# Performance work log

Hardware: AMD Instinct MI355X
Metric: run time of the kernel (lower is better)

The kernel has to match this reference:

```python
import jax, jax.numpy as jnp
import numpy as np

BETA = 1.0
B, N, D = 2048, 131072, 256

def setup_inputs() -> dict:
    key = jax.random.key(0)
    k1, k2 = jax.random.split(key)
    x = jax.random.normal(k1, (B, D), dtype=jnp.float32)
    stored = jax.random.normal(k2, (N, D), dtype=jnp.float32)
    return {"x": x, "stored": stored}

def reference(x, stored):
    # scores: [B, N] = beta * x @ stored^T
    scores = BETA * jnp.einsum('bd,nd->bn', x, stored)
    attn = jax.nn.softmax(scores, axis=-1)
    # retrieved patterns: [B, D]
    return jnp.einsum('bn,nd->bd', attn, stored)
```

## Files before the change

### kernel.cpp

```cpp
#include <hip/hip_runtime.h>
#include <hip/hip_bf16.h>
#include <math.h>

#define B_Q 2048
#define N_K 131072
#define D_DIM 256
#define NCHUNK 32
#define CHUNK_KEYS (N_K / NCHUNK)
#define KTILE 32
#define NITER (CHUNK_KEYS / KTILE)
#define NTILES (N_K / KTILE)
#define TILE_USHORTS 16384

typedef __attribute__((ext_vector_type(8))) _Float16 half8;
typedef __attribute__((ext_vector_type(8))) short bf16x8;
typedef __attribute__((ext_vector_type(4))) float f32x4;

static __device__ __forceinline__ unsigned short f2bf(float f) {
    unsigned u = __builtin_bit_cast(unsigned, f);
    unsigned r = (u + 0x7fffu + ((u >> 16) & 1u)) >> 16;
    return (unsigned short)r;
}

typedef const __attribute__((address_space(1))) unsigned int* gas_p;
typedef __attribute__((address_space(3))) unsigned int* las_p;
static __device__ __forceinline__ void gl_lds16(const void* g, void* l) {
    __builtin_amdgcn_global_load_lds((gas_p)g, (las_p)l, 16, 0, 0);
}

__global__ __launch_bounds__(256) void prepass(const float* __restrict__ stored,
                                               unsigned short* __restrict__ frag) {
    __shared__ float sh[32][270];
    const int tid = threadIdx.x;
    const int t = blockIdx.x;
    const float* src = stored + (size_t)t * 32 * 256;
#pragma unroll
    for (int i = 0; i < 16; ++i) {
        int gi = i * 256 + tid;
        int row = gi >> 7, c2 = (gi & 127) << 1;
        *(float2*)&sh[row][c2] = *(const float2*)(src + row * 256 + c2);
    }
    __syncthreads();
    unsigned short* out = frag + (size_t)t * TILE_USHORTS;
#pragma unroll
    for (int i = 0; i < 4; ++i) {
        int ck = i * 256 + tid;
        int lane = ck & 63, col = lane & 15, quad = lane >> 4;
        int kg = ck >> 9, s = (ck >> 6) & 7;
        int key = kg * 16 + col, d0 = s * 32 + quad * 8;
        union { uint4 v; _Float16 e[8]; } o;
#pragma unroll
        for (int j2 = 0; j2 < 4; ++j2) {
            float2 f = *(const float2*)&sh[key][d0 + j2 * 2];
            o.e[j2 * 2]     = (_Float16)f.x;
            o.e[j2 * 2 + 1] = (_Float16)f.y;
        }
        *(uint4*)(out + ck * 8) = o.v;
    }
#pragma unroll
    for (int i = 0; i < 4; ++i) {
        int cv = i * 256 + tid;
        int lane = cv & 63, col = lane & 15, quad = lane >> 4;
        int dn = cv >> 6;
        int d = dn * 16 + col;
        union { uint4 v; unsigned short e[8]; } o;
#pragma unroll
        for (int j = 0; j < 8; ++j) o.e[j] = f2bf(sh[quad * 8 + j][d]);
        *(uint4*)(out + 8192 + cv * 8) = o.v;
    }
}

__global__ __launch_bounds__(256, 2)
void hopfield_main(const float* __restrict__ x,
                   const unsigned short* __restrict__ frag,
                   float* __restrict__ partO,
                   float* __restrict__ partl) {
    __shared__ __align__(16) unsigned short Kb[2][8192];
    __shared__ __align__(16) unsigned short Vb[2][8192];
    __shared__ __align__(16) unsigned short Pb[4][32][40];

    const int tid = threadIdx.x;
    const int wave = tid >> 6, lane = tid & 63;
    const int col = lane & 15, quad = lane >> 4;
    const int blk = blockIdx.x;
    const int chunk = blk & 31, qb = blk >> 5;
    const int q0w = qb * 128 + wave * 32;
    const unsigned short* fbase = frag + (size_t)chunk * NITER * TILE_USHORTS;

    half8 xf[2][8];
    float ss[2] = {0.f, 0.f};
#pragma unroll
    for (int qg = 0; qg < 2; ++qg) {
        const float* xr = x + (size_t)(q0w + qg * 16 + col) * 256;
#pragma unroll
        for (int s = 0; s < 8; ++s) {
            f32x4 a = *(const f32x4*)(xr + s * 32 + quad * 8);
            f32x4 b = *(const f32x4*)(xr + s * 32 + quad * 8 + 4);
            union { half8 v; _Float16 e[8]; } h;
#pragma unroll
            for (int j = 0; j < 4; ++j) {
                h.e[j] = (_Float16)a[j]; h.e[4 + j] = (_Float16)b[j];
                ss[qg] += a[j] * a[j] + b[j] * b[j];
            }
            xf[qg][s] = h.v;
        }
    }
#pragma unroll
    for (int qg = 0; qg < 2; ++qg) {
        ss[qg] += __shfl_xor(ss[qg], 16);
        ss[qg] += __shfl_xor(ss[qg], 32);
    }
    float M0q[2] = {4.9f * sqrtf(ss[0]), 4.9f * sqrtf(ss[1])};
    float M0v[2][4];
#pragma unroll
    for (int qg = 0; qg < 2; ++qg)
#pragma unroll
        for (int r = 0; r < 4; ++r)
            M0v[qg][r] = __shfl(M0q[qg], quad * 4 + r);

    f32x4 O[2][16];
#pragma unroll
    for (int qg = 0; qg < 2; ++qg)
#pragma unroll
        for (int dn = 0; dn < 16; ++dn) O[qg][dn] = (f32x4){0.f, 0.f, 0.f, 0.f};
    float lacc[2][4] = {{0.f, 0.f, 0.f, 0.f}, {0.f, 0.f, 0.f, 0.f}};

#pragma unroll
    for (int j = 0; j < 4; ++j) {
        int off = (wave * 4 + j) * 512 + lane * 8;
        gl_lds16(fbase + off, &Kb[0][off]);
        gl_lds16(fbase + 8192 + off, &Vb[0][off]);
    }

#pragma unroll 1
    for (int it = 0; it < NITER; ++it) {
        const int cur = it & 1;
        __syncthreads();

        const int itn = (it + 1 < NITER) ? it + 1 : it;
        const unsigned short* nbase = fbase + (size_t)itn * TILE_USHORTS;
#pragma unroll
        for (int j = 0; j < 4; ++j) {
            int off = (wave * 4 + j) * 512 + lane * 8;
            gl_lds16(nbase + off, &Kb[itn & 1][off]);
            gl_lds16(nbase + 8192 + off, &Vb[itn & 1][off]);
        }

        const unsigned short* K = Kb[cur];
        const unsigned short* V = Vb[cur];

        f32x4 S[2][2];
#pragma unroll
        for (int qg = 0; qg < 2; ++qg)
#pragma unroll
            for (int kg = 0; kg < 2; ++kg) S[qg][kg] = (f32x4){0.f, 0.f, 0.f, 0.f};
#pragma unroll
        for (int s = 0; s < 8; ++s) {
            half8 b0 = *(const half8*)(K + ((0 * 8 + s) * 64 + lane) * 8);
            half8 b1 = *(const half8*)(K + ((1 * 8 + s) * 64 + lane) * 8);
            S[0][0] = __builtin_amdgcn_mfma_f32_16x16x32_f16(xf[0][s], b0, S[0][0], 0, 0, 0);
            S[1][0] = __builtin_amdgcn_mfma_f32_16x16x32_f16(xf[1][s], b0, S[1][0], 0, 0, 0);
            S[0][1] = __builtin_amdgcn_mfma_f32_16x16x32_f16(xf[0][s], b1, S[0][1], 0, 0, 0);
            S[1][1] = __builtin_amdgcn_mfma_f32_16x16x32_f16(xf[1][s], b1, S[1][1], 0, 0, 0);
        }

        unsigned short* Pw = &Pb[wave][0][0];
#pragma unroll
        for (int qg = 0; qg < 2; ++qg)
#pragma unroll
            for (int r = 0; r < 4; ++r) {
                float m0 = M0v[qg][r];
                float p0 = __expf(S[qg][0][r] - m0);
                float p1 = __expf(S[qg][1][r] - m0);
                lacc[qg][r] += p0 + p1;
                int row = qg * 16 + quad * 4 + r;
                Pw[row * 40 + col]      = f2bf(p0);
                Pw[row * 40 + 16 + col] = f2bf(p1);
            }
        asm volatile("s_waitcnt lgkmcnt(0)" ::: "memory");
        bf16x8 pa[2];
#pragma unroll
        for (int qg = 0; qg < 2; ++qg)
            pa[qg] = *(const bf16x8*)&Pb[wave][qg * 16 + col][quad * 8];

#pragma unroll
        for (int dn = 0; dn < 16; ++dn) {
            bf16x8 bv = *(const bf16x8*)(V + (dn * 64 + lane) * 8);
            O[0][dn] = __builtin_amdgcn_mfma_f32_16x16x32_bf16(pa[0], bv, O[0][dn], 0, 0, 0);
            O[1][dn] = __builtin_amdgcn_mfma_f32_16x16x32_bf16(pa[1], bv, O[1][dn], 0, 0, 0);
        }
    }

#pragma unroll
    for (int qg = 0; qg < 2; ++qg)
#pragma unroll
        for (int r = 0; r < 4; ++r) {
            float v = lacc[qg][r];
            v += __shfl_xor(v, 1); v += __shfl_xor(v, 2);
            v += __shfl_xor(v, 4); v += __shfl_xor(v, 8);
            if (col == 0)
                partl[(size_t)chunk * B_Q + q0w + qg * 16 + quad * 4 + r] = v;
        }
#pragma unroll
    for (int qg = 0; qg < 2; ++qg)
#pragma unroll
        for (int dn = 0; dn < 16; ++dn)
#pragma unroll
            for (int r = 0; r < 4; ++r) {
                int q = q0w + qg * 16 + quad * 4 + r;
                partO[((size_t)chunk * B_Q + q) * 256 + dn * 16 + col] = O[qg][dn][r];
            }
}

__global__ void combine_kernel(const float* __restrict__ partO,
                               const float* __restrict__ partl,
                               float* __restrict__ out) {
    const int q = blockIdx.x;
    const int d = threadIdx.x;
    float L = 0.f;
#pragma unroll
    for (int c = 0; c < NCHUNK; ++c) L += partl[(size_t)c * B_Q + q];
    float acc = 0.f;
#pragma unroll
    for (int c = 0; c < NCHUNK; ++c)
        acc += partO[((size_t)c * B_Q + q) * 256 + d];
    out[(size_t)q * 256 + d] = acc / L;
}

extern "C" void kernel_launch(void* const* d_in, const int* in_sizes, int n_in,
                              void* d_out, int out_size, void* d_ws, size_t ws_size,
                              hipStream_t stream) {
    const float* x      = (const float*)d_in[0];
    const float* stored = (const float*)d_in[1];
    float* out = (float*)d_out;

    char* wsb = (char*)d_ws;
    unsigned short* frag = (unsigned short*)wsb;
    float* partO = (float*)(wsb + (size_t)134217728);
    float* partl = (float*)(wsb + (size_t)134217728 + 67108864);

    prepass<<<NTILES, 256, 0, stream>>>(stored, frag);
    hopfield_main<<<512, 256, 0, stream>>>(x, frag, partO, partl);
    combine_kernel<<<B_Q, 256, 0, stream>>>(partO, partl, out);
}
```

Baseline: 490.2 us.

## Read K fragments directly from global, software-pipeline PV MFMA across iterations

The K tile is no longer staged through LDS; each wave loads its K fragments straight from global memory, which halves LDS traffic and footprint. The P·V MFMA for the previous tile is deferred to the start of the next iteration so it overlaps with the next QK computation. P values are written as packed pairs with an interleaved key order, matched by a permuted V layout in the prepass. The prepass also moves to 512 threads per block. The trade-off is more global/L2 load latency exposed on the QK path, and the explicit lgkmcnt wait before the P readback is removed, which relies on compiler-inserted waits for correctness.

```diff
diff --git a/kernel.cpp b/kernel.cpp
--- a/kernel.cpp
+++ b/kernel.cpp
@@ -28,23 +28,23 @@
     __builtin_amdgcn_global_load_lds((gas_p)g, (las_p)l, 16, 0, 0);
 }
 
-__global__ __launch_bounds__(256) void prepass(const float* __restrict__ stored,
+__global__ __launch_bounds__(512) void prepass(const float* __restrict__ stored,
                                                unsigned short* __restrict__ frag) {
     __shared__ float sh[32][270];
     const int tid = threadIdx.x;
     const int t = blockIdx.x;
     const float* src = stored + (size_t)t * 32 * 256;
 #pragma unroll
-    for (int i = 0; i < 16; ++i) {
-        int gi = i * 256 + tid;
+    for (int i = 0; i < 8; ++i) {
+        int gi = i * 512 + tid;
         int row = gi >> 7, c2 = (gi & 127) << 1;
         *(float2*)&sh[row][c2] = *(const float2*)(src + row * 256 + c2);
     }
     __syncthreads();
     unsigned short* out = frag + (size_t)t * TILE_USHORTS;
 #pragma unroll
-    for (int i = 0; i < 4; ++i) {
-        int ck = i * 256 + tid;
+    for (int i = 0; i < 2; ++i) {
+        int ck = i * 512 + tid;
         int lane = ck & 63, col = lane & 15, quad = lane >> 4;
         int kg = ck >> 9, s = (ck >> 6) & 7;
         int key = kg * 16 + col, d0 = s * 32 + quad * 8;
@@ -58,14 +58,18 @@
         *(uint4*)(out + ck * 8) = o.v;
     }
 #pragma unroll
-    for (int i = 0; i < 4; ++i) {
-        int cv = i * 256 + tid;
+    for (int i = 0; i < 2; ++i) {
+        int cv = i * 512 + tid;
         int lane = cv & 63, col = lane & 15, quad = lane >> 4;
         int dn = cv >> 6;
         int d = dn * 16 + col;
         union { uint4 v; unsigned short e[8]; } o;
 #pragma unroll
-        for (int j = 0; j < 8; ++j) o.e[j] = f2bf(sh[quad * 8 + j][d]);
+        for (int j = 0; j < 8; ++j) {
+            int pos = quad * 8 + j;
+            int key = (pos & 1) * 16 + (pos >> 1);
+            o.e[j] = f2bf(sh[key][d]);
+        }
         *(uint4*)(out + 8192 + cv * 8) = o.v;
     }
 }
@@ -75,7 +79,6 @@
                    const unsigned short* __restrict__ frag,
                    float* __restrict__ partO,
                    float* __restrict__ partl) {
-    __shared__ __align__(16) unsigned short Kb[2][8192];
     __shared__ __align__(16) unsigned short Vb[2][8192];
     __shared__ __align__(16) unsigned short Pb[4][32][40];
 
@@ -124,31 +127,38 @@
 #pragma unroll
         for (int dn = 0; dn < 16; ++dn) O[qg][dn] = (f32x4){0.f, 0.f, 0.f, 0.f};
     float lacc[2][4] = {{0.f, 0.f, 0.f, 0.f}, {0.f, 0.f, 0.f, 0.f}};
+    bf16x8 pa[2];
+    pa[0] = (bf16x8){0,0,0,0,0,0,0,0};
+    pa[1] = (bf16x8){0,0,0,0,0,0,0,0};
 
 #pragma unroll
     for (int j = 0; j < 4; ++j) {
         int off = (wave * 4 + j) * 512 + lane * 8;
-        gl_lds16(fbase + off, &Kb[0][off]);
         gl_lds16(fbase + 8192 + off, &Vb[0][off]);
     }
 
 #pragma unroll 1
     for (int it = 0; it < NITER; ++it) {
-        const int cur = it & 1;
+        if (it) {
+            const unsigned short* V = Vb[(it + 1) & 1];
+#pragma unroll
+            for (int dn = 0; dn < 16; ++dn) {
+                bf16x8 bv = *(const bf16x8*)(V + (dn * 64 + lane) * 8);
+                O[0][dn] = __builtin_amdgcn_mfma_f32_16x16x32_bf16(pa[0], bv, O[0][dn], 0, 0, 0);
+                O[1][dn] = __builtin_amdgcn_mfma_f32_16x16x32_bf16(pa[1], bv, O[1][dn], 0, 0, 0);
+            }
+        }
         __syncthreads();
 
         const int itn = (it + 1 < NITER) ? it + 1 : it;
-        const unsigned short* nbase = fbase + (size_t)itn * TILE_USHORTS;
+        const unsigned short* nb = fbase + (size_t)itn * TILE_USHORTS + 8192;
 #pragma unroll
         for (int j = 0; j < 4; ++j) {
             int off = (wave * 4 + j) * 512 + lane * 8;
-            gl_lds16(nbase + off, &Kb[itn & 1][off]);
-            gl_lds16(nbase + 8192 + off, &Vb[itn & 1][off]);
-        }
-
-        const unsigned short* K = Kb[cur];
-        const unsigned short* V = Vb[cur];
-
+            gl_lds16(nb + off, &Vb[itn & 1][off]);
+        }
+
+        const unsigned short* Kt = fbase + (size_t)it * TILE_USHORTS;
         f32x4 S[2][2];
 #pragma unroll
         for (int qg = 0; qg < 2; ++qg)
@@ -156,8 +166,8 @@
             for (int kg = 0; kg < 2; ++kg) S[qg][kg] = (f32x4){0.f, 0.f, 0.f, 0.f};
 #pragma unroll
         for (int s = 0; s < 8; ++s) {
-            half8 b0 = *(const half8*)(K + ((0 * 8 + s) * 64 + lane) * 8);
-            half8 b1 = *(const half8*)(K + ((1 * 8 + s) * 64 + lane) * 8);
+            half8 b0 = *(const half8*)(Kt + ((size_t)(s * 64 + lane)) * 8);
+            half8 b1 = *(const half8*)(Kt + ((size_t)((8 + s) * 64 + lane)) * 8);
             S[0][0] = __builtin_amdgcn_mfma_f32_16x16x32_f16(xf[0][s], b0, S[0][0], 0, 0, 0);
             S[1][0] = __builtin_amdgcn_mfma_f32_16x16x32_f16(xf[1][s], b0, S[1][0], 0, 0, 0);
             S[0][1] = __builtin_amdgcn_mfma_f32_16x16x32_f16(xf[0][s], b1, S[0][1], 0, 0, 0);
@@ -174,15 +184,16 @@
                 float p1 = __expf(S[qg][1][r] - m0);
                 lacc[qg][r] += p0 + p1;
                 int row = qg * 16 + quad * 4 + r;
-                Pw[row * 40 + col]      = f2bf(p0);
-                Pw[row * 40 + 16 + col] = f2bf(p1);
-            }
-        asm volatile("s_waitcnt lgkmcnt(0)" ::: "memory");
-        bf16x8 pa[2];
+                unsigned pk = (unsigned)f2bf(p0) | ((unsigned)f2bf(p1) << 16);
+                *(unsigned*)(Pw + row * 40 + 2 * col) = pk;
+            }
 #pragma unroll
         for (int qg = 0; qg < 2; ++qg)
             pa[qg] = *(const bf16x8*)&Pb[wave][qg * 16 + col][quad * 8];
-
+    }
+
+    {
+        const unsigned short* V = Vb[(NITER - 1) & 1];
 #pragma unroll
         for (int dn = 0; dn < 16; ++dn) {
             bf16x8 bv = *(const bf16x8*)(V + (dn * 64 + lane) * 8);
@@ -239,7 +250,7 @@
     float* partO = (float*)(wsb + (size_t)134217728);
     float* partl = (float*)(wsb + (size_t)134217728 + 67108864);
 
-    prepass<<<NTILES, 256, 0, stream>>>(stored, frag);
+    prepass<<<NTILES, 512, 0, stream>>>(stored, frag);
     hopfield_main<<<512, 256, 0, stream>>>(x, frag, partO, partl);
     combine_kernel<<<B_Q, 256, 0, stream>>>(partO, partl, out);
 }
```

Result: slower. 646.0 us (+31.8%).
